# Kernel optimization log

Hardware: AMD Instinct MI355X
Metric: run time of the kernel (lower is better)

The kernel has to match this reference:

```python
import jax, jax.numpy as jnp
import numpy as np

N = 100000      # nodes
E = 1600000     # edges (before self-loops)
F_IN = 128      # num_node_features
H = 8           # heads in conv1
C = 16          # per-head channels in conv1 (hard-coded in module)
K = 32          # num_classes (conv2 out, single head)
NEG_SLOPE = 0.2 # PyG GATConv default


def setup_inputs() -> dict:
    key = jax.random.key(0)
    ks = jax.random.split(key, 8)
    x = jax.random.normal(ks[0], (N, F_IN), dtype=jnp.float32)
    edge_index = jax.random.randint(ks[1], (2, E), 0, N, dtype=jnp.int32)
    # conv1 params (Glorot-ish scale)
    W1 = jax.random.normal(ks[2], (H * C, F_IN), dtype=jnp.float32) / np.sqrt(F_IN)
    att_src1 = jax.random.normal(ks[3], (H, C), dtype=jnp.float32) / np.sqrt(C)
    att_dst1 = jax.random.normal(ks[4], (H, C), dtype=jnp.float32) / np.sqrt(C)
    b1 = jnp.zeros((H * C,), dtype=jnp.float32)
    # conv2 params (heads=1)
    W2 = jax.random.normal(ks[5], (K, H * C), dtype=jnp.float32) / np.sqrt(H * C)
    att_src2 = jax.random.normal(ks[6], (1, K), dtype=jnp.float32) / np.sqrt(K)
    att_dst2 = jax.random.normal(ks[7], (1, K), dtype=jnp.float32) / np.sqrt(K)
    b2 = jnp.zeros((K,), dtype=jnp.float32)
    return {"inputs": x, "edge_index": edge_index,
            "W1": W1, "att_src1": att_src1, "att_dst1": att_dst1, "b1": b1,
            "W2": W2, "att_src2": att_src2, "att_dst2": att_dst2, "b2": b2}


def gat_conv(x, src, dst, W, a_src, a_dst, bias, heads, ch):
    # x: [N, F_in]; src/dst: [E2] (self-loops already appended)
    h = (x @ W.T).reshape(N, heads, ch)                  # [N, H, C]
    al_s = (h * a_src[None]).sum(-1)                     # [N, H]
    al_d = (h * a_dst[None]).sum(-1)                     # [N, H]
    e = al_s[src] + al_d[dst]                            # [E2, H]
    e = jnp.where(e >= 0, e, NEG_SLOPE * e)              # LeakyReLU
    # segment softmax over edges sharing a destination node
    m = jax.ops.segment_max(e, dst, num_segments=N)      # [N, H]
    p = jnp.exp(e - m[dst])
    s = jax.ops.segment_sum(p, dst, num_segments=N)
    alpha = p / (s[dst] + 1e-16)                         # [E2, H]
    msg = h[src] * alpha[:, :, None]                     # [E2, H, C]
    out = jax.ops.segment_sum(msg, dst, num_segments=N)  # [N, H, C]
    return out.reshape(N, heads * ch) + bias, alpha


def reference(inputs, edge_index, W1, att_src1, att_dst1, b1, W2, att_src2, att_dst2, b2):
    loop = jnp.arange(N, dtype=edge_index.dtype)
    src = jnp.concatenate([edge_index[0], loop])         # add self-loops
    dst = jnp.concatenate([edge_index[1], loop])
    x1, _ = gat_conv(inputs, src, dst, W1, att_src1, att_dst1, b1, H, C)
    x1 = jax.nn.relu(x1)                                 # [N, H*C]
    x2, alpha = gat_conv(x1, src, dst, W2, att_src2, att_dst2, b2, 1, K)
    edge_index_new = jnp.stack([src, dst])               # [2, E+N]
    return x2, edge_index_new, alpha
```

## Files before the change

### kernel.cpp

```cpp
#include <hip/hip_runtime.h>
#include <hip/hip_bf16.h>
#include <cstdint>
#include <cstddef>

#define NN  100000
#define EE  1600000
#define NE2 1700000
#define NBINS 391
#define NREP  8
#define BCAP  1024
#define EPB   4096
#define NBINBLK 416
#define NG1BLK  1563

#define OUT_X2    3200000
#define OUT_ALPHA 6600000

__device__ __forceinline__ float lrelu(float v) { return v >= 0.f ? v : 0.2f * v; }

typedef float v2f __attribute__((ext_vector_type(2)));
typedef short short8 __attribute__((ext_vector_type(8)));
typedef float f32x4 __attribute__((ext_vector_type(4)));

__device__ __forceinline__ unsigned cvtpk_bf16(float lo, float hi) {
  unsigned r;
  asm("v_cvt_pk_bf16_f32 %0, %1, %2" : "=v"(r) : "v"(lo), "v"(hi));
  return r;
}

#if __has_builtin(__builtin_amdgcn_cvt_pk_f32_fp8) && __has_builtin(__builtin_amdgcn_cvt_pk_fp8_f32)
#define HW_FP8 1
#endif

__device__ __forceinline__ float fp8dec1(unsigned b) {
  unsigned e = (b >> 3) & 15, m = b & 7;
  float v = e ? __uint_as_float(((e + 120u) << 23) | (m << 20))
              : (float)m * 0.001953125f;
  return (b & 0x80u) ? -v : v;
}
__device__ __forceinline__ unsigned fp8enc1(float x) {
  unsigned s = x < 0.f ? 0x80u : 0u;
  float a = fminf(fabsf(x), 448.f);
  if (a < 0.0009765625f) return s;
  unsigned ub = __float_as_uint(a);
  int ex = (int)(ub >> 23) - 127;
  if (ex < -6) {
    unsigned m = (unsigned)(a * 512.f + 0.5f);
    return s | (m > 7u ? 7u : m);
  }
  float sc = __uint_as_float((unsigned)(127 - ex) << 23);
  unsigned m = (unsigned)((a * sc - 1.f) * 8.f + 0.5f);
  if (m == 8u) { m = 0u; ++ex; }
  if (ex > 8) { ex = 8; m = 7u; }
  return s | ((unsigned)(ex + 7) << 3) | m;
}

template <bool HI>
__device__ __forceinline__ v2f fp8x2(unsigned u) {
#ifdef HW_FP8
  return __builtin_amdgcn_cvt_pk_f32_fp8((int)u, HI);
#else
  unsigned w = HI ? (u >> 16) : u;
  v2f r; r.x = fp8dec1(w & 255u); r.y = fp8dec1((w >> 8) & 255u);
  return r;
#endif
}
__device__ __forceinline__ unsigned packfp8x4(float a, float b, float c, float d) {
#ifdef HW_FP8
  int r = __builtin_amdgcn_cvt_pk_fp8_f32(a, b, 0, false);
  r = __builtin_amdgcn_cvt_pk_fp8_f32(c, d, r, true);
  return (unsigned)r;
#else
  return fp8enc1(a) | (fp8enc1(b) << 8) | (fp8enc1(c) << 16) | (fp8enc1(d) << 24);
#endif
}

__device__ __forceinline__ void acc16(float w, uint4 u,
    float4& A, float4& B, float4& C, float4& D)
{
  v2f p;
  p = fp8x2<false>(u.x); A.x += w * p.x; A.y += w * p.y;
  p = fp8x2<true >(u.x); A.z += w * p.x; A.w += w * p.y;
  p = fp8x2<false>(u.y); B.x += w * p.x; B.y += w * p.y;
  p = fp8x2<true >(u.y); B.z += w * p.x; B.w += w * p.y;
  p = fp8x2<false>(u.z); C.x += w * p.x; C.y += w * p.y;
  p = fp8x2<true >(u.z); C.z += w * p.x; C.w += w * p.y;
  p = fp8x2<false>(u.w); D.x += w * p.x; D.y += w * p.y;
  p = fp8x2<true >(u.w); D.z += w * p.x; D.w += w * p.y;
}

__global__ __launch_bounds__(256) void k_bin_gemm1(
    const int* __restrict__ ei, int* __restrict__ bincnt,
    unsigned* __restrict__ binbuf, float* __restrict__ out,
    const float* __restrict__ x, const float* __restrict__ W1,
    const float* __restrict__ a_src, const float* __restrict__ a_dst,
    unsigned* __restrict__ h1f8, float* __restrict__ als, float* __restrict__ ald)
{
  __shared__ __align__(16) char lds[49152];
  const int t = threadIdx.x;

  if (blockIdx.x < NBINBLK) {
    int* hist  = (int*)lds;
    int* bbase = hist + NBINS;
    const int e0 = blockIdx.x * EPB;
    const int rep = blockIdx.x & (NREP - 1);
    int* bc = bincnt + rep * NBINS;
    unsigned* bb = binbuf + (size_t)rep * NBINS * BCAP;

    int mybin[16];
    unsigned mypay[16];

    for (int i = t; i < NBINS; i += 256) hist[i] = 0;
    __syncthreads();

    #pragma unroll
    for (int k = 0; k < 16; ++k) {
      int i = e0 + k * 256 + t;
      int b = -1; unsigned pay = 0;
      if (i < NE2) {
        int src, dst;
        if (i < EE) { src = ei[i]; dst = ei[EE + i]; } else { src = dst = i - EE; }
        out[OUT_X2 + i] = (float)src;
        out[OUT_X2 + NE2 + i] = (float)dst;
        b = dst >> 8;
        pay = ((unsigned)src << 8) | (dst & 255);
        atomicAdd(&hist[b], 1);
      }
      mybin[k] = b; mypay[k] = pay;
    }
    __syncthreads();

    for (int i = t; i < NBINS; i += 256) {
      int c = hist[i];
      bbase[i] = c ? atomicAdd(&bc[i], c) : 0;
      hist[i] = 0;
    }
    __syncthreads();

    #pragma unroll
    for (int k = 0; k < 16; ++k) {
      int b = mybin[k];
      if (b >= 0) {
        int pos = bbase[b] + atomicAdd(&hist[b], 1);
        if (pos < BCAP) bb[(size_t)b * BCAP + pos] = mypay[k];
      }
    }
    return;
  }

  char* xs_c = lds;
  char* Wb_c = lds + 16384;
  float* Cl  = (float*)lds;
  const int row0 = (blockIdx.x - NBINBLK) * 64;

  #pragma unroll
  for (int i = 0; i < 16; ++i) {
    int idx4 = i * 256 + t;
    int n = idx4 >> 5, kq = idx4 & 31;
    float4 v = ((const float4*)W1)[idx4];
    unsigned lo = cvtpk_bf16(v.x, v.y), hi = cvtpk_bf16(v.z, v.w);
    int byte = n * 256 + ((((kq >> 1) ^ (n & 7)) << 4) | ((kq & 1) << 3));
    *(uint2*)(Wb_c + byte) = make_uint2(lo, hi);
  }
  #pragma unroll
  for (int i = 0; i < 8; ++i) {
    int idx4 = i * 256 + t;
    int r = idx4 >> 5, kq = idx4 & 31;
    int grow = row0 + r;
    float4 v = (grow < NN) ? ((const float4*)x)[(size_t)grow * 32 + kq]
                           : make_float4(0.f, 0.f, 0.f, 0.f);
    unsigned lo = cvtpk_bf16(v.x, v.y), hi = cvtpk_bf16(v.z, v.w);
    int byte = r * 256 + ((((kq >> 1) ^ (r & 7)) << 4) | ((kq & 1) << 3));
    *(uint2*)(xs_c + byte) = make_uint2(lo, hi);
  }
  __syncthreads();

  const int w = t >> 6, l = t & 63, m = l & 15, g = l >> 4;
  f32x4 acc[8] = {};
  const char* xrow = xs_c + (16 * w + m) * 256;
  #pragma unroll
  for (int kk = 0; kk < 4; ++kk) {
    int chunk = (((kk << 2) + g) ^ (m & 7)) << 4;
    short8 av = *(const short8*)(xrow + chunk);
    #pragma unroll
    for (int nb = 0; nb < 8; ++nb) {
      short8 bv = *(const short8*)(Wb_c + (16 * nb + m) * 256 + chunk);
      acc[nb] = __builtin_amdgcn_mfma_f32_16x16x32_bf16(av, bv, acc[nb], 0, 0, 0);
    }
  }

  __syncthreads();
  #pragma unroll
  for (int nb = 0; nb < 8; ++nb)
    #pragma unroll
    for (int j = 0; j < 4; ++j)
      Cl[(16 * w + 4 * g + j) * 128 + 16 * nb + m] = acc[nb][j];
  __syncthreads();

  const int cg = t & 31, rg = t >> 5;
  float4 sA = ((const float4*)a_src)[cg];
  float4 dA = ((const float4*)a_dst)[cg];
  #pragma unroll
  for (int j = 0; j < 8; ++j) {
    int r = 8 * rg + j;
    int grow = row0 + r;
    if (grow >= NN) break;
    float4 cv = *(const float4*)&Cl[r * 128 + 4 * cg];
    h1f8[(size_t)grow * 32 + cg] = packfp8x4(cv.x, cv.y, cv.z, cv.w);
    float ps = cv.x * sA.x + cv.y * sA.y + cv.z * sA.z + cv.w * sA.w;
    float pd = cv.x * dA.x + cv.y * dA.y + cv.z * dA.z + cv.w * dA.w;
    ps += __shfl_xor(ps, 1); ps += __shfl_xor(ps, 2);
    pd += __shfl_xor(pd, 1); pd += __shfl_xor(pd, 2);
    if ((cg & 3) == 0) {
      als[(size_t)grow * 8 + (cg >> 2)] = ps;
      ald[(size_t)grow * 8 + (cg >> 2)] = pd;
    }
  }
}

__global__ __launch_bounds__(256) void k_binsort(
    const unsigned* __restrict__ binbuf, const int* __restrict__ bincnt,
    int* __restrict__ base, int* __restrict__ csr)
{
  __shared__ int deg[256];
  __shared__ int sc[256];
  __shared__ int cur[256];
  const int b = blockIdx.x;
  const int t = threadIdx.x;

  int acc = 0;
  #pragma unroll
  for (int r = 0; r < NREP; ++r)
    for (int i = t; i < b; i += 256)
      acc += bincnt[r * NBINS + i];
  deg[t] = acc;
  __syncthreads();
  #pragma unroll
  for (int off = 128; off >= 1; off >>= 1) {
    if (t < off) deg[t] += deg[t + off];
    __syncthreads();
  }
  const int start = deg[0];
  __syncthreads();

  deg[t] = 0;
  __syncthreads();
  #pragma unroll
  for (int r = 0; r < NREP; ++r) {
    int cnt = bincnt[r * NBINS + b];
    const unsigned* buf = binbuf + (size_t)(r * NBINS + b) * BCAP;
    for (int i = t; i < cnt; i += 256)
      atomicAdd(&deg[buf[i] & 255], 1);
  }
  __syncthreads();

  sc[t] = deg[t];
  __syncthreads();
  #pragma unroll
  for (int off = 1; off < 256; off <<= 1) {
    int add = (t >= off) ? sc[t - off] : 0;
    __syncthreads();
    sc[t] += add;
    __syncthreads();
  }
  int excl = sc[t] - deg[t];

  int node = b * 256 + t;
  if (node < NN) base[node] = start + excl;
  if (b == NBINS - 1 && t == 0) base[NN] = NE2;
  cur[t] = excl;
  __syncthreads();

  #pragma unroll
  for (int r = 0; r < NREP; ++r) {
    int cnt = bincnt[r * NBINS + b];
    const unsigned* buf = binbuf + (size_t)(r * NBINS + b) * BCAP;
    for (int i = t; i < cnt; i += 256) {
      unsigned u = buf[i];
      int pos = atomicAdd(&cur[u & 255], 1);
      csr[start + pos] = (int)(u >> 8);
    }
  }
}

__global__ __launch_bounds__(256) void k_node1(
    const int* __restrict__ base, const int* __restrict__ csr_src,
    const float* __restrict__ als, const float* __restrict__ ald,
    const uint4* __restrict__ h1x4, uint4* __restrict__ acc1x4)
{
  int gid = blockIdx.x * 256 + threadIdx.x;
  int node = gid >> 3;
  int q = gid & 7;
  float ad = ald[(size_t)node * 8 + q];
  int s0 = base[node], s1 = base[node + 1];
  float4 A = {0,0,0,0}, B = {0,0,0,0}, C = {0,0,0,0}, D = {0,0,0,0};
  float sw = 0.f;
  int i = s0;
  int n4 = s0 + ((s1 - s0) & ~3);
  int c0 = 0, c1 = 0, c2 = 0, c3 = 0;
  if (i < n4) {
    c0 = csr_src[i]; c1 = csr_src[i + 1];
    c2 = csr_src[i + 2]; c3 = csr_src[i + 3];
  }
  while (i < n4) {
    int src0 = c0, src1 = c1, src2 = c2, src3 = c3;
    int ni = i + 4;
    if (ni < n4) {
      c0 = csr_src[ni]; c1 = csr_src[ni + 1];
      c2 = csr_src[ni + 2]; c3 = csr_src[ni + 3];
    }
    float e0 = als[(size_t)src0 * 8 + q] + ad;
    float e1 = als[(size_t)src1 * 8 + q] + ad;
    float e2 = als[(size_t)src2 * 8 + q] + ad;
    float e3 = als[(size_t)src3 * 8 + q] + ad;
    uint4 u0 = h1x4[(size_t)src0 * 8 + q];
    uint4 u1 = h1x4[(size_t)src1 * 8 + q];
    uint4 u2 = h1x4[(size_t)src2 * 8 + q];
    uint4 u3 = h1x4[(size_t)src3 * 8 + q];
    float w0 = __expf(lrelu(e0));
    float w1 = __expf(lrelu(e1));
    float w2 = __expf(lrelu(e2));
    float w3 = __expf(lrelu(e3));
    acc16(w0, u0, A, B, C, D);
    acc16(w1, u1, A, B, C, D);
    acc16(w2, u2, A, B, C, D);
    acc16(w3, u3, A, B, C, D);
    sw += w0 + w1 + w2 + w3;
    i = ni;
  }
  for (; i < s1; ++i) {
    int src = csr_src[i];
    float w = __expf(lrelu(als[(size_t)src * 8 + q] + ad));
    uint4 u = h1x4[(size_t)src * 8 + q];
    acc16(w, u, A, B, C, D);
    sw += w;
  }
  float inv = 1.f / (sw + 1e-16f);
  uint4 o;
  o.x = packfp8x4(A.x * inv, A.y * inv, A.z * inv, A.w * inv);
  o.y = packfp8x4(B.x * inv, B.y * inv, B.z * inv, B.w * inv);
  o.z = packfp8x4(C.x * inv, C.y * inv, C.z * inv, C.w * inv);
  o.w = packfp8x4(D.x * inv, D.y * inv, D.z * inv, D.w * inv);
  acc1x4[(size_t)node * 8 + q] = o;
}

__global__ __launch_bounds__(256) void k_gemm2(
    const unsigned* __restrict__ acc1f8, const float* __restrict__ b1,
    const float* __restrict__ W2, const float* __restrict__ a_src,
    const float* __restrict__ a_dst,
    unsigned* __restrict__ h2f8, float* __restrict__ als, float* __restrict__ ald)
{
  __shared__ float Wt[128 * 32];
  __shared__ float xs[64 * 132];
  const int t = threadIdx.x;
  const int row0 = blockIdx.x * 64;

  {
    const float4* W4 = (const float4*)W2;
    #pragma unroll
    for (int i = 0; i < 4; ++i) {
      int idx4 = t * 4 + i;
      int c = idx4 >> 5, f4 = idx4 & 31;
      float4 v = W4[idx4];
      Wt[(4 * f4 + 0) * 32 + c] = v.x;
      Wt[(4 * f4 + 1) * 32 + c] = v.y;
      Wt[(4 * f4 + 2) * 32 + c] = v.z;
      Wt[(4 * f4 + 3) * 32 + c] = v.w;
    }
  }
  #pragma unroll
  for (int i = 0; i < 8; ++i) {
    int idx = i * 256 + t;
    int r = idx >> 5, u = idx & 31;
    int grow = row0 + r;
    unsigned v = (grow < NN) ? acc1f8[(size_t)grow * 32 + u] : 0u;
    float4 bb = ((const float4*)b1)[u];
    v2f lo = fp8x2<false>(v), hi = fp8x2<true>(v);
    xs[r * 132 + 4 * u + 0] = fmaxf(lo.x + bb.x, 0.f);
    xs[r * 132 + 4 * u + 1] = fmaxf(lo.y + bb.y, 0.f);
    xs[r * 132 + 4 * u + 2] = fmaxf(hi.x + bb.z, 0.f);
    xs[r * 132 + 4 * u + 3] = fmaxf(hi.y + bb.w, 0.f);
  }
  __syncthreads();

  const int c4 = t & 7;
  const int rg = t >> 3;
  float acc[2][4];
  #pragma unroll
  for (int j = 0; j < 2; ++j)
    #pragma unroll
    for (int k = 0; k < 4; ++k) acc[j][k] = 0.f;

  const float4* Wt4 = (const float4*)Wt;
  #pragma unroll 4
  for (int f = 0; f < 128; ++f) {
    float4 wv = Wt4[f * 8 + c4];
    #pragma unroll
    for (int j = 0; j < 2; ++j) {
      float xv = xs[(2 * rg + j) * 132 + f];
      acc[j][0] += xv * wv.x; acc[j][1] += xv * wv.y;
      acc[j][2] += xv * wv.z; acc[j][3] += xv * wv.w;
    }
  }

  float4 sv = ((const float4*)a_src)[c4];
  float4 dv = ((const float4*)a_dst)[c4];
  #pragma unroll
  for (int j = 0; j < 2; ++j) {
    int grow = row0 + 2 * rg + j;
    if (grow < NN) {
      h2f8[(size_t)grow * 8 + c4] = packfp8x4(acc[j][0], acc[j][1], acc[j][2], acc[j][3]);
      float ps = acc[j][0] * sv.x + acc[j][1] * sv.y + acc[j][2] * sv.z + acc[j][3] * sv.w;
      float pd = acc[j][0] * dv.x + acc[j][1] * dv.y + acc[j][2] * dv.z + acc[j][3] * dv.w;
      ps += __shfl_xor(ps, 1); ps += __shfl_xor(ps, 2); ps += __shfl_xor(ps, 4);
      pd += __shfl_xor(pd, 1); pd += __shfl_xor(pd, 2); pd += __shfl_xor(pd, 4);
      if (c4 == 0) { als[grow] = ps; ald[grow] = pd; }
    }
  }
}

__global__ __launch_bounds__(256) void k_node2(
    const int* __restrict__ base, const int* __restrict__ csr_src,
    const float* __restrict__ als, const float* __restrict__ ald,
    const uint2* __restrict__ h2x2, const float* __restrict__ b2,
    float* __restrict__ out_x2, float* __restrict__ s2)
{
  int gid = blockIdx.x * 256 + threadIdx.x;
  int node = gid >> 2, j = gid & 3;
  if (node >= NN) return;
  float ad = ald[node];
  int s0 = base[node], s1 = base[node + 1];
  float4 A = {0,0,0,0}, B = {0,0,0,0};
  float sw = 0.f;
  int i = s0;
  int n4 = s0 + ((s1 - s0) & ~3);
  for (; i < n4; i += 4) {
    int src0 = csr_src[i + 0];
    int src1 = csr_src[i + 1];
    int src2 = csr_src[i + 2];
    int src3 = csr_src[i + 3];
    float e0 = als[src0] + ad;
    float e1 = als[src1] + ad;
    float e2 = als[src2] + ad;
    float e3 = als[src3] + ad;
    uint2 u0 = h2x2[(size_t)src0 * 4 + j];
    uint2 u1 = h2x2[(size_t)src1 * 4 + j];
    uint2 u2 = h2x2[(size_t)src2 * 4 + j];
    uint2 u3 = h2x2[(size_t)src3 * 4 + j];
    float w0 = __expf(lrelu(e0));
    float w1 = __expf(lrelu(e1));
    float w2 = __expf(lrelu(e2));
    float w3 = __expf(lrelu(e3));
    { v2f p;
      p = fp8x2<false>(u0.x); A.x += w0 * p.x; A.y += w0 * p.y;
      p = fp8x2<true >(u0.x); A.z += w0 * p.x; A.w += w0 * p.y;
      p = fp8x2<false>(u0.y); B.x += w0 * p.x; B.y += w0 * p.y;
      p = fp8x2<true >(u0.y); B.z += w0 * p.x; B.w += w0 * p.y; }
    { v2f p;
      p = fp8x2<false>(u1.x); A.x += w1 * p.x; A.y += w1 * p.y;
      p = fp8x2<true >(u1.x); A.z += w1 * p.x; A.w += w1 * p.y;
      p = fp8x2<false>(u1.y); B.x += w1 * p.x; B.y += w1 * p.y;
      p = fp8x2<true >(u1.y); B.z += w1 * p.x; B.w += w1 * p.y; }
    { v2f p;
      p = fp8x2<false>(u2.x); A.x += w2 * p.x; A.y += w2 * p.y;
      p = fp8x2<true >(u2.x); A.z += w2 * p.x; A.w += w2 * p.y;
      p = fp8x2<false>(u2.y); B.x += w2 * p.x; B.y += w2 * p.y;
      p = fp8x2<true >(u2.y); B.z += w2 * p.x; B.w += w2 * p.y; }
    { v2f p;
      p = fp8x2<false>(u3.x); A.x += w3 * p.x; A.y += w3 * p.y;
      p = fp8x2<true >(u3.x); A.z += w3 * p.x; A.w += w3 * p.y;
      p = fp8x2<false>(u3.y); B.x += w3 * p.x; B.y += w3 * p.y;
      p = fp8x2<true >(u3.y); B.z += w3 * p.x; B.w += w3 * p.y; }
    sw += w0 + w1 + w2 + w3;
  }
  for (; i < s1; ++i) {
    int src = csr_src[i];
    float w = __expf(lrelu(als[src] + ad));
    uint2 u = h2x2[(size_t)src * 4 + j];
    v2f p;
    p = fp8x2<false>(u.x); A.x += w * p.x; A.y += w * p.y;
    p = fp8x2<true >(u.x); A.z += w * p.x; A.w += w * p.y;
    p = fp8x2<false>(u.y); B.x += w * p.x; B.y += w * p.y;
    p = fp8x2<true >(u.y); B.z += w * p.x; B.w += w * p.y;
    sw += w;
  }
  float inv = 1.f / (sw + 1e-16f);
  float4 b0 = ((const float4*)b2)[2 * j];
  float4 b1v = ((const float4*)b2)[2 * j + 1];
  float4* o = (float4*)&out_x2[(size_t)node * 32 + 8 * j];
  o[0] = make_float4(A.x * inv + b0.x, A.y * inv + b0.y,
                     A.z * inv + b0.z, A.w * inv + b0.w);
  o[1] = make_float4(B.x * inv + b1v.x, B.y * inv + b1v.y,
                     B.z * inv + b1v.z, B.w * inv + b1v.w);
  if (j == 0) s2[node] = sw;
}

__global__ __launch_bounds__(256) void k_alpha_edges(
    const int* __restrict__ ei, const float* __restrict__ als,
    const float* __restrict__ ald, const float* __restrict__ s2,
    float* __restrict__ out)
{
  int e = blockIdx.x * 256 + threadIdx.x;
  if (e >= NE2) return;
  int src, dst;
  if (e < EE) { src = ei[e]; dst = ei[EE + e]; } else { src = dst = e - EE; }
  float w = __expf(lrelu(als[src] + ald[dst]));
  out[OUT_ALPHA + e] = w / (s2[dst] + 1e-16f);
}

extern "C" void kernel_launch(void* const* d_in, const int* in_sizes, int n_in,
                              void* d_out, int out_size, void* d_ws, size_t ws_size,
                              hipStream_t stream)
{
  const float* x   = (const float*)d_in[0];
  const int*   ei  = (const int*)d_in[1];
  const float* W1  = (const float*)d_in[2];
  const float* as1 = (const float*)d_in[3];
  const float* ad1 = (const float*)d_in[4];
  const float* b1  = (const float*)d_in[5];
  const float* W2  = (const float*)d_in[6];
  const float* as2 = (const float*)d_in[7];
  const float* ad2 = (const float*)d_in[8];
  const float* b2  = (const float*)d_in[9];
  float* out = (float*)d_out;

  if (ws_size < 60000000) return;

  char* ws = (char*)d_ws;
  unsigned* h1f8    = (unsigned*)(ws + 0);
  unsigned* acc1f8  = (unsigned*)(ws + 12800000);
  float*    als1    = (float*)(ws + 25600000);
  float*    ald1    = (float*)(ws + 28800000);
  unsigned* h2f8    = (unsigned*)(ws + 32000000);
  float*    als2    = (float*)(ws + 35200000);
  float*    ald2    = (float*)(ws + 35600000);
  float*    s2      = (float*)(ws + 36000000);
  int*      bincnt  = (int*)(ws + 36400000);
  int*      base    = (int*)(ws + 36416384);
  int*      csr     = (int*)(ws + 36816388);
  unsigned* binbuf  = (unsigned*)(ws + 43616388);

  (void)hipMemsetAsync(bincnt, 0, NREP * NBINS * 4, stream);

  k_bin_gemm1<<<NBINBLK + NG1BLK, 256, 0, stream>>>(
      ei, bincnt, binbuf, out, x, W1, as1, ad1, h1f8, als1, ald1);

  k_binsort<<<NBINS, 256, 0, stream>>>(binbuf, bincnt, base, csr);

  k_node1<<<(NN * 8) / 256, 256, 0, stream>>>(base, csr, als1, ald1,
                                              (const uint4*)h1f8, (uint4*)acc1f8);

  k_gemm2<<<(NN + 63) / 64, 256, 0, stream>>>(acc1f8, b1, W2, as2, ad2, h2f8, als2, ald2);
  k_node2<<<(NN * 4 + 255) / 256, 256, 0, stream>>>(base, csr, als2, ald2,
                                                    (const uint2*)h2f8, b2, out, s2);

  k_alpha_edges<<<(NE2 + 255) / 256, 256, 0, stream>>>(ei, als2, ald2, s2, out);
}
```

Before: 179.3 us.

## Fuse layer-1 aggregation with layer-2 linear transform in one kernel

```diff
diff --git a/kernel.cpp b/kernel.cpp
--- a/kernel.cpp
+++ b/kernel.cpp
@@ -283,14 +283,23 @@
   }
 }
 
-__global__ __launch_bounds__(256) void k_node1(
+__global__ __launch_bounds__(256) void k_node1_gemm2(
     const int* __restrict__ base, const int* __restrict__ csr_src,
     const float* __restrict__ als, const float* __restrict__ ald,
-    const uint4* __restrict__ h1x4, uint4* __restrict__ acc1x4)
-{
-  int gid = blockIdx.x * 256 + threadIdx.x;
-  int node = gid >> 3;
-  int q = gid & 7;
+    const uint4* __restrict__ h1x4, const float* __restrict__ b1,
+    const float* __restrict__ W2, const float* __restrict__ a_src2,
+    const float* __restrict__ a_dst2,
+    unsigned* __restrict__ h2f8, float* __restrict__ als2, float* __restrict__ ald2)
+{
+  __shared__ float xs[32 * 132];
+  __shared__ float Wt[128 * 32];
+
+  const int t = threadIdx.x;
+  const int node0 = blockIdx.x * 32;
+  const int nl = t >> 3;
+  const int q = t & 7;
+  const int node = node0 + nl;
+
   float ad = ald[(size_t)node * 8 + q];
   int s0 = base[node], s1 = base[node + 1];
   float4 A = {0,0,0,0}, B = {0,0,0,0}, C = {0,0,0,0}, D = {0,0,0,0};
@@ -336,30 +345,33 @@
     sw += w;
   }
   float inv = 1.f / (sw + 1e-16f);
-  uint4 o;
-  o.x = packfp8x4(A.x * inv, A.y * inv, A.z * inv, A.w * inv);
-  o.y = packfp8x4(B.x * inv, B.y * inv, B.z * inv, B.w * inv);
-  o.z = packfp8x4(C.x * inv, C.y * inv, C.z * inv, C.w * inv);
-  o.w = packfp8x4(D.x * inv, D.y * inv, D.z * inv, D.w * inv);
-  acc1x4[(size_t)node * 8 + q] = o;
-}
-
-__global__ __launch_bounds__(256) void k_gemm2(
-    const unsigned* __restrict__ acc1f8, const float* __restrict__ b1,
-    const float* __restrict__ W2, const float* __restrict__ a_src,
-    const float* __restrict__ a_dst,
-    unsigned* __restrict__ h2f8, float* __restrict__ als, float* __restrict__ ald)
-{
-  __shared__ float Wt[128 * 32];
-  __shared__ float xs[64 * 132];
-  const int t = threadIdx.x;
-  const int row0 = blockIdx.x * 64;
-
+
+  {
+    float* row = &xs[nl * 132 + 16 * q];
+    const float4* bb = (const float4*)&b1[16 * q];
+    float4 b0 = bb[0], b1v = bb[1], b2v = bb[2], b3v = bb[3];
+    row[0]  = fmaxf(A.x * inv + b0.x, 0.f);
+    row[1]  = fmaxf(A.y * inv + b0.y, 0.f);
+    row[2]  = fmaxf(A.z * inv + b0.z, 0.f);
+    row[3]  = fmaxf(A.w * inv + b0.w, 0.f);
+    row[4]  = fmaxf(B.x * inv + b1v.x, 0.f);
+    row[5]  = fmaxf(B.y * inv + b1v.y, 0.f);
+    row[6]  = fmaxf(B.z * inv + b1v.z, 0.f);
+    row[7]  = fmaxf(B.w * inv + b1v.w, 0.f);
+    row[8]  = fmaxf(C.x * inv + b2v.x, 0.f);
+    row[9]  = fmaxf(C.y * inv + b2v.y, 0.f);
+    row[10] = fmaxf(C.z * inv + b2v.z, 0.f);
+    row[11] = fmaxf(C.w * inv + b2v.w, 0.f);
+    row[12] = fmaxf(D.x * inv + b3v.x, 0.f);
+    row[13] = fmaxf(D.y * inv + b3v.y, 0.f);
+    row[14] = fmaxf(D.z * inv + b3v.z, 0.f);
+    row[15] = fmaxf(D.w * inv + b3v.w, 0.f);
+  }
   {
     const float4* W4 = (const float4*)W2;
     #pragma unroll
-    for (int i = 0; i < 4; ++i) {
-      int idx4 = t * 4 + i;
+    for (int ii = 0; ii < 4; ++ii) {
+      int idx4 = ii * 256 + t;
       int c = idx4 >> 5, f4 = idx4 & 31;
       float4 v = W4[idx4];
       Wt[(4 * f4 + 0) * 32 + c] = v.x;
@@ -368,55 +380,25 @@
       Wt[(4 * f4 + 3) * 32 + c] = v.w;
     }
   }
-  #pragma unroll
-  for (int i = 0; i < 8; ++i) {
-    int idx = i * 256 + t;
-    int r = idx >> 5, u = idx & 31;
-    int grow = row0 + r;
-    unsigned v = (grow < NN) ? acc1f8[(size_t)grow * 32 + u] : 0u;
-    float4 bb = ((const float4*)b1)[u];
-    v2f lo = fp8x2<false>(v), hi = fp8x2<true>(v);
-    xs[r * 132 + 4 * u + 0] = fmaxf(lo.x + bb.x, 0.f);
-    xs[r * 132 + 4 * u + 1] = fmaxf(lo.y + bb.y, 0.f);
-    xs[r * 132 + 4 * u + 2] = fmaxf(hi.x + bb.z, 0.f);
-    xs[r * 132 + 4 * u + 3] = fmaxf(hi.y + bb.w, 0.f);
-  }
-  __syncthreads();
-
-  const int c4 = t & 7;
-  const int rg = t >> 3;
-  float acc[2][4];
-  #pragma unroll
-  for (int j = 0; j < 2; ++j)
-    #pragma unroll
-    for (int k = 0; k < 4; ++k) acc[j][k] = 0.f;
-
+  __syncthreads();
+
+  float g0 = 0.f, g1 = 0.f, g2 = 0.f, g3 = 0.f;
+  const float* xrow = &xs[nl * 132];
   const float4* Wt4 = (const float4*)Wt;
   #pragma unroll 4
   for (int f = 0; f < 128; ++f) {
-    float4 wv = Wt4[f * 8 + c4];
-    #pragma unroll
-    for (int j = 0; j < 2; ++j) {
-      float xv = xs[(2 * rg + j) * 132 + f];
-      acc[j][0] += xv * wv.x; acc[j][1] += xv * wv.y;
-      acc[j][2] += xv * wv.z; acc[j][3] += xv * wv.w;
-    }
-  }
-
-  float4 sv = ((const float4*)a_src)[c4];
-  float4 dv = ((const float4*)a_dst)[c4];
-  #pragma unroll
-  for (int j = 0; j < 2; ++j) {
-    int grow = row0 + 2 * rg + j;
-    if (grow < NN) {
-      h2f8[(size_t)grow * 8 + c4] = packfp8x4(acc[j][0], acc[j][1], acc[j][2], acc[j][3]);
-      float ps = acc[j][0] * sv.x + acc[j][1] * sv.y + acc[j][2] * sv.z + acc[j][3] * sv.w;
-      float pd = acc[j][0] * dv.x + acc[j][1] * dv.y + acc[j][2] * dv.z + acc[j][3] * dv.w;
-      ps += __shfl_xor(ps, 1); ps += __shfl_xor(ps, 2); ps += __shfl_xor(ps, 4);
-      pd += __shfl_xor(pd, 1); pd += __shfl_xor(pd, 2); pd += __shfl_xor(pd, 4);
-      if (c4 == 0) { als[grow] = ps; ald[grow] = pd; }
-    }
-  }
+    float xv = xrow[f];
+    float4 wv = Wt4[f * 8 + q];
+    g0 += xv * wv.x; g1 += xv * wv.y; g2 += xv * wv.z; g3 += xv * wv.w;
+  }
+  h2f8[(size_t)node * 8 + q] = packfp8x4(g0, g1, g2, g3);
+  float4 sv = ((const float4*)a_src2)[q];
+  float4 dv = ((const float4*)a_dst2)[q];
+  float ps = g0 * sv.x + g1 * sv.y + g2 * sv.z + g3 * sv.w;
+  float pd = g0 * dv.x + g1 * dv.y + g2 * dv.z + g3 * dv.w;
+  ps += __shfl_xor(ps, 1); ps += __shfl_xor(ps, 2); ps += __shfl_xor(ps, 4);
+  pd += __shfl_xor(pd, 1); pd += __shfl_xor(pd, 2); pd += __shfl_xor(pd, 4);
+  if (q == 0) { als2[node] = ps; ald2[node] = pd; }
 }
 
 __global__ __launch_bounds__(256) void k_node2(
@@ -528,17 +510,16 @@
 
   char* ws = (char*)d_ws;
   unsigned* h1f8    = (unsigned*)(ws + 0);
-  unsigned* acc1f8  = (unsigned*)(ws + 12800000);
-  float*    als1    = (float*)(ws + 25600000);
-  float*    ald1    = (float*)(ws + 28800000);
-  unsigned* h2f8    = (unsigned*)(ws + 32000000);
-  float*    als2    = (float*)(ws + 35200000);
-  float*    ald2    = (float*)(ws + 35600000);
-  float*    s2      = (float*)(ws + 36000000);
-  int*      bincnt  = (int*)(ws + 36400000);
-  int*      base    = (int*)(ws + 36416384);
-  int*      csr     = (int*)(ws + 36816388);
-  unsigned* binbuf  = (unsigned*)(ws + 43616388);
+  unsigned* h2f8    = (unsigned*)(ws + 12800000);
+  float*    als1    = (float*)(ws + 16000000);
+  float*    ald1    = (float*)(ws + 19200000);
+  float*    als2    = (float*)(ws + 22400000);
+  float*    ald2    = (float*)(ws + 22800000);
+  float*    s2      = (float*)(ws + 23200000);
+  int*      bincnt  = (int*)(ws + 23600000);
+  int*      base    = (int*)(ws + 23616384);
+  int*      csr     = (int*)(ws + 24016388);
+  unsigned* binbuf  = (unsigned*)(ws + 30816388);
 
   (void)hipMemsetAsync(bincnt, 0, NREP * NBINS * 4, stream);
 
@@ -547,12 +528,11 @@
 
   k_binsort<<<NBINS, 256, 0, stream>>>(binbuf, bincnt, base, csr);
 
-  k_node1<<<(NN * 8) / 256, 256, 0, stream>>>(base, csr, als1, ald1,
-                                              (const uint4*)h1f8, (uint4*)acc1f8);
-
-  k_gemm2<<<(NN + 63) / 64, 256, 0, stream>>>(acc1f8, b1, W2, as2, ad2, h2f8, als2, ald2);
+  k_node1_gemm2<<<NN / 32, 256, 0, stream>>>(base, csr, als1, ald1,
+                                             (const uint4*)h1f8, b1, W2,
+                                             as2, ad2, h2f8, als2, ald2);
+
   k_node2<<<(NN * 4 + 255) / 256, 256, 0, stream>>>(base, csr, als2, ald2,
                                                     (const uint2*)h2f8, b2, out, s2);
-
   k_alpha_edges<<<(NE2 + 255) / 256, 256, 0, stream>>>(ei, als2, ald2, s2, out);
 }
```

After: 189.6 us. 1.06x slower.
